# Kernel optimization log

Hardware: AMD Instinct MI355X
Metric: run time of the kernel (lower is better)

Reference implementation:

```python
import jax, jax.numpy as jnp
import numpy as np

N = 8192       # nodes
IN_F = 512     # in_features
OUT_F = 256    # out_features


def setup_inputs() -> dict:
    key = jax.random.key(0)
    k1, k2, k3, k4 = jax.random.split(key, 4)
    # xavier_uniform-like scales for params
    w_scale = 1.414 * (6.0 / (IN_F + OUT_F)) ** 0.5
    a_scale = 1.414 * (6.0 / (2 * OUT_F + 1)) ** 0.5
    x = jax.random.normal(k1, (N, IN_F), jnp.float32)
    W = jax.random.uniform(k2, (IN_F, OUT_F), jnp.float32, -w_scale, w_scale)
    a = jax.random.uniform(k3, (2 * OUT_F, 1), jnp.float32, -a_scale, a_scale)
    adj = jax.random.randint(k4, (N, N), 0, 2, jnp.int32)
    return {"x": x, "W": W, "a": a, "adj": adj}


def reference(x, W, a, adj):
    # h = x @ W : [N, OUT_F]
    h = x @ W
    f = W.shape[1]
    a1, a2 = a[:f], a[f:]          # each [OUT_F, 1]
    # Original builds a_input[i,j] = concat(h_i, h_j) then matmuls with a.
    # Equivalent decomposition: e[i,j] = h_i . a1 + h_j . a2
    e = (h @ a1) + (h @ a2).T      # [N, N]
    neg = jnp.float32(-9e15)
    attention = jnp.where(adj > 0, e, neg)   # no softmax in the original
    h_prime = attention @ h        # [N, OUT_F]
    return h_prime
```

## Files before the change

### kernel.cpp

```cpp
#include <hip/hip_runtime.h>


#define NEG_BIG (-9000000000000000.0f)
#define POS_BIG (9000000000000000.0f)

typedef __bf16 bf16x8 __attribute__((ext_vector_type(8)));
typedef float f32x16 __attribute__((ext_vector_type(16)));

static __device__ __forceinline__ unsigned short f2bf(float f) {
  unsigned u = __builtin_bit_cast(unsigned, f);
  u = u + 0x7FFFu + ((u >> 16) & 1u);
  return (unsigned short)(u >> 16);
}
static __device__ __forceinline__ float bfbits2f(unsigned hi16) {
  return __builtin_bit_cast(float, hi16 << 16);
}
static __device__ __forceinline__ unsigned pk2(float a, float b) {
  return (unsigned)f2bf(a) | ((unsigned)f2bf(b) << 16);
}
static __device__ __forceinline__ unsigned m2(int a, int b) {
  return (unsigned)(a + (b << 16)) * 0x3F80u;
}
static __device__ __forceinline__ bf16x8 asbf(int4 q) {
  return __builtin_bit_cast(bf16x8, q);
}
static __device__ __forceinline__ bf16x8 mfrag(int4 u, int4 v) {
  union { unsigned w[4]; bf16x8 f; } r;
  r.w[0] = m2(u.x, u.y); r.w[1] = m2(u.z, u.w);
  r.w[2] = m2(v.x, v.y); r.w[3] = m2(v.z, v.w);
  return r.f;
}
static __device__ __forceinline__ f32x16 mfma(bf16x8 a, int4 b, f32x16 c) {
  return __builtin_amdgcn_mfma_f32_32x32x16_bf16(a, asbf(b), c, 0, 0, 0);
}

__global__ void k1a_wt(const float* __restrict__ W, unsigned short* __restrict__ WT,
                       float* __restrict__ T) {
  const int i = blockIdx.x * 256 + threadIdx.x;
  const int k = i >> 8, n = i & 255;
  WT[n * 512 + k] = f2bf(W[i]);
  if (blockIdx.x == 0) T[threadIdx.x] = 0.f;
}

__global__ __launch_bounds__(256) void k1b_h(const float* __restrict__ x,
    const unsigned short* __restrict__ WT, unsigned short* __restrict__ hP) {
  const int t = threadIdx.x;
  const int w = t >> 6, l = t & 63, l31 = l & 31, lh = l >> 5;
  const int gw = blockIdx.x * 4 + w;
  const int mt = gw >> 3, nt = gw & 7;
  const int m0 = mt << 5, n0 = nt << 5;
  f32x16 acc;
  for (int i = 0; i < 16; ++i) acc[i] = 0.f;
  const float* xr = x + (size_t)(m0 + l31) * 512 + lh * 8;
  const unsigned short* wr = WT + (size_t)(n0 + l31) * 512 + lh * 8;
#pragma unroll 4
  for (int k0 = 0; k0 < 512; k0 += 16) {
    float4 xa = *(const float4*)(xr + k0);
    float4 xb = *(const float4*)(xr + k0 + 4);
    int4 wb = *(const int4*)(wr + k0);
    union { unsigned u[4]; bf16x8 v; } A;
    A.u[0] = pk2(xa.x, xa.y); A.u[1] = pk2(xa.z, xa.w);
    A.u[2] = pk2(xb.x, xb.y); A.u[3] = pk2(xb.z, xb.w);
    acc = __builtin_amdgcn_mfma_f32_32x32x16_bf16(A.v, asbf(wb), acc, 0, 0, 0);
  }
#pragma unroll
  for (int reg = 0; reg < 16; ++reg) {
    const int m = m0 + (reg & 3) + 8 * (reg >> 2) + 4 * lh;
    const int n = n0 + l31;
    hP[(size_t)(m >> 5) * 8192 + n * 32 + (m & 31)] = f2bf(acc[reg]);
  }
}

__global__ __launch_bounds__(256) void k2_colsum(const unsigned short* __restrict__ hP,
                                                 float* __restrict__ T) {
  const int t = threadIdx.x;
  const int g = blockIdx.x;
  float s = 0.f;
#pragma unroll
  for (int b = 0; b < 8; ++b) {
    const int4* p = (const int4*)(hP + (size_t)(g * 8 + b) * 8192 + t * 32);
    int4 q0 = p[0], q1 = p[1], q2 = p[2], q3 = p[3];
    const unsigned* u = (const unsigned*)&q0;
#pragma unroll
    for (int i = 0; i < 4; ++i) s += bfbits2f(u[i] & 0xFFFFu) + bfbits2f(u[i] >> 16);
    u = (const unsigned*)&q1;
#pragma unroll
    for (int i = 0; i < 4; ++i) s += bfbits2f(u[i] & 0xFFFFu) + bfbits2f(u[i] >> 16);
    u = (const unsigned*)&q2;
#pragma unroll
    for (int i = 0; i < 4; ++i) s += bfbits2f(u[i] & 0xFFFFu) + bfbits2f(u[i] >> 16);
    u = (const unsigned*)&q3;
#pragma unroll
    for (int i = 0; i < 4; ++i) s += bfbits2f(u[i] & 0xFFFFu) + bfbits2f(u[i] >> 16);
  }
  atomicAdd(&T[t], s);
}

__global__ void k2b_init(const float* __restrict__ T, float* __restrict__ out) {
  const int i = blockIdx.x * 256 + threadIdx.x;
  const int n4 = (i & 63) * 4;
  float4 tv = *(const float4*)(T + n4);
  float4 o;
  o.x = NEG_BIG * tv.x; o.y = NEG_BIG * tv.y;
  o.z = NEG_BIG * tv.z; o.w = NEG_BIG * tv.w;
  ((float4*)out)[i] = o;
}

__global__ __launch_bounds__(256, 4) void k3_att(const int* __restrict__ adj,
    const unsigned short* __restrict__ hP, float* __restrict__ out) {
  const int t = threadIdx.x;
  const int blk = blockIdx.x;
  const int s = blk & 7;
  const int rt = blk >> 3;
  const int w = t >> 6;
  const int l = t & 63;
  const int l31 = l & 31;
  const int lh = l >> 5;
  const int n0 = w << 6;

  const int r0 = rt * 64 + l31;
  const int* aR0 = adj + (size_t)r0 * 8192 + s * 1024 + lh * 8;
  const int* aR1 = aR0 + (size_t)32 * 8192;
  const unsigned short* hB = hP + (size_t)(s * 32) * 8192 + (n0 + l31) * 32 + lh * 8;

  f32x16 a00, a01, a10, a11;
  for (int i = 0; i < 16; ++i) { a00[i] = 0.f; a01[i] = 0.f; a10[i] = 0.f; a11[i] = 0.f; }

  for (int it = 0; it < 32; ++it) {
    const int4* q0 = (const int4*)(aR0 + it * 32);
    const int4* q1 = (const int4*)(aR1 + it * 32);
    const unsigned short* hb = hB + (size_t)it * 8192;
    int4 b00 = *(const int4*)(hb);
    int4 b01 = *(const int4*)(hb + 16);
    int4 b10 = *(const int4*)(hb + 1024);
    int4 b11 = *(const int4*)(hb + 1040);
    int4 u00a = q0[0], u00b = q0[1];
    int4 u10a = q1[0], u10b = q1[1];
    bf16x8 A00 = mfrag(u00a, u00b);
    bf16x8 A10 = mfrag(u10a, u10b);
    a00 = mfma(A00, b00, a00);
    a01 = mfma(A00, b10, a01);
    a10 = mfma(A10, b00, a10);
    a11 = mfma(A10, b10, a11);
    int4 u01a = q0[4], u01b = q0[5];
    int4 u11a = q1[4], u11b = q1[5];
    bf16x8 A01 = mfrag(u01a, u01b);
    bf16x8 A11 = mfrag(u11a, u11b);
    a00 = mfma(A01, b01, a00);
    a01 = mfma(A01, b11, a01);
    a10 = mfma(A11, b01, a10);
    a11 = mfma(A11, b11, a11);
  }

  const int rb0 = rt * 64 + 4 * lh;
  const int nn = n0 + l31;
#pragma unroll
  for (int reg = 0; reg < 16; ++reg) {
    const int ro = (reg & 3) + 8 * (reg >> 2);
    float* p = out + (size_t)(rb0 + ro) * 256 + nn;
    atomicAdd(p, POS_BIG * a00[reg]);
    atomicAdd(p + 32, POS_BIG * a01[reg]);
    float* p2 = p + 32 * 256;
    atomicAdd(p2, POS_BIG * a10[reg]);
    atomicAdd(p2 + 32, POS_BIG * a11[reg]);
  }
}

extern "C" void kernel_launch(void* const* d_in, const int* in_sizes, int n_in,
                              void* d_out, int out_size, void* d_ws, size_t ws_size,
                              hipStream_t stream) {
  const float* x = (const float*)d_in[0];
  const float* W = (const float*)d_in[1];
  const int* adj = (const int*)d_in[3];
  float* out = (float*)d_out;
  char* ws = (char*)d_ws;
  unsigned short* WT = (unsigned short*)(ws);
  unsigned short* hP = (unsigned short*)(ws + (1 << 20));
  float* T = (float*)(ws + (6 << 20));

  k1a_wt<<<512, 256, 0, stream>>>(W, WT, T);
  k1b_h<<<512, 256, 0, stream>>>(x, WT, hP);
  k2_colsum<<<32, 256, 0, stream>>>(hP, T);
  k2b_init<<<2048, 256, 0, stream>>>(T, out);
  k3_att<<<1024, 256, 0, stream>>>(adj, hP, out);
}
```

Before: 530.7 us.

## Stage adjacency tiles through double-buffered LDS in attention kernel, widen colsum grid

The attention kernel stops having each wave load and convert its own adjacency fragments from global memory. All threads now cooperatively load 64x64 adjacency tiles with coalesced loads, convert them once to bf16, and write them into a padded, double-buffered shared-memory tile that the waves read as MFMA A-fragments. The next tile is prefetched while MFMAs run on the current one. This removes the redundant global reads and conversions that the four waves each did for the same rows, at the cost of one barrier per iteration and extra LDS use that may limit occupancy. Separately, the column-sum kernel now uses one block per row-block, 256 blocks instead of 32, which increases parallelism but also the number of atomic adds.

```diff
diff --git a/kernel.cpp b/kernel.cpp
--- a/kernel.cpp
+++ b/kernel.cpp
@@ -23,12 +23,6 @@
 }
 static __device__ __forceinline__ bf16x8 asbf(int4 q) {
   return __builtin_bit_cast(bf16x8, q);
-}
-static __device__ __forceinline__ bf16x8 mfrag(int4 u, int4 v) {
-  union { unsigned w[4]; bf16x8 f; } r;
-  r.w[0] = m2(u.x, u.y); r.w[1] = m2(u.z, u.w);
-  r.w[2] = m2(v.x, v.y); r.w[3] = m2(v.z, v.w);
-  return r.f;
 }
 static __device__ __forceinline__ f32x16 mfma(bf16x8 a, int4 b, f32x16 c) {
   return __builtin_amdgcn_mfma_f32_32x32x16_bf16(a, asbf(b), c, 0, 0, 0);
@@ -74,24 +68,20 @@
 __global__ __launch_bounds__(256) void k2_colsum(const unsigned short* __restrict__ hP,
                                                  float* __restrict__ T) {
   const int t = threadIdx.x;
-  const int g = blockIdx.x;
+  const int b = blockIdx.x;
+  const int4* p = (const int4*)(hP + (size_t)b * 8192 + t * 32);
+  int4 q0 = p[0], q1 = p[1], q2 = p[2], q3 = p[3];
   float s = 0.f;
-#pragma unroll
-  for (int b = 0; b < 8; ++b) {
-    const int4* p = (const int4*)(hP + (size_t)(g * 8 + b) * 8192 + t * 32);
-    int4 q0 = p[0], q1 = p[1], q2 = p[2], q3 = p[3];
-    const unsigned* u = (const unsigned*)&q0;
-#pragma unroll
-    for (int i = 0; i < 4; ++i) s += bfbits2f(u[i] & 0xFFFFu) + bfbits2f(u[i] >> 16);
-    u = (const unsigned*)&q1;
-#pragma unroll
-    for (int i = 0; i < 4; ++i) s += bfbits2f(u[i] & 0xFFFFu) + bfbits2f(u[i] >> 16);
-    u = (const unsigned*)&q2;
-#pragma unroll
-    for (int i = 0; i < 4; ++i) s += bfbits2f(u[i] & 0xFFFFu) + bfbits2f(u[i] >> 16);
-    u = (const unsigned*)&q3;
-#pragma unroll
-    for (int i = 0; i < 4; ++i) s += bfbits2f(u[i] & 0xFFFFu) + bfbits2f(u[i] >> 16);
+  const unsigned* u0 = (const unsigned*)&q0;
+  const unsigned* u1 = (const unsigned*)&q1;
+  const unsigned* u2 = (const unsigned*)&q2;
+  const unsigned* u3 = (const unsigned*)&q3;
+#pragma unroll
+  for (int i = 0; i < 4; ++i) {
+    s += bfbits2f(u0[i] & 0xFFFFu) + bfbits2f(u0[i] >> 16);
+    s += bfbits2f(u1[i] & 0xFFFFu) + bfbits2f(u1[i] >> 16);
+    s += bfbits2f(u2[i] & 0xFFFFu) + bfbits2f(u2[i] >> 16);
+    s += bfbits2f(u3[i] & 0xFFFFu) + bfbits2f(u3[i] >> 16);
   }
   atomicAdd(&T[t], s);
 }
@@ -106,8 +96,10 @@
   ((float4*)out)[i] = o;
 }
 
+#define LSTR 68
 __global__ __launch_bounds__(256, 4) void k3_att(const int* __restrict__ adj,
     const unsigned short* __restrict__ hP, float* __restrict__ out) {
+  __shared__ unsigned short A[2][64 * LSTR];
   const int t = threadIdx.x;
   const int blk = blockIdx.x;
   const int s = blk & 7;
@@ -118,38 +110,71 @@
   const int lh = l >> 5;
   const int n0 = w << 6;
 
-  const int r0 = rt * 64 + l31;
-  const int* aR0 = adj + (size_t)r0 * 8192 + s * 1024 + lh * 8;
-  const int* aR1 = aR0 + (size_t)32 * 8192;
-  const unsigned short* hB = hP + (size_t)(s * 32) * 8192 + (n0 + l31) * 32 + lh * 8;
+  const int srow = t >> 4;
+  const int scol = (t & 15) << 2;
+  const int* aBase = adj + (size_t)(rt * 64 + srow) * 8192 + s * 1024 + scol;
+  unsigned short* const wA0 = &A[0][srow * LSTR + scol];
+  unsigned short* const wA1 = &A[1][srow * LSTR + scol];
+
+  const int fr0 = l31 * (LSTR * 2) + lh * 16;
+  const int fr1 = fr0 + 32 * (LSTR * 2);
+
+  const unsigned short* hB = hP + (n0 + l31) * 32 + lh * 8;
 
   f32x16 a00, a01, a10, a11;
   for (int i = 0; i < 16; ++i) { a00[i] = 0.f; a01[i] = 0.f; a10[i] = 0.f; a11[i] = 0.f; }
 
-  for (int it = 0; it < 32; ++it) {
-    const int4* q0 = (const int4*)(aR0 + it * 32);
-    const int4* q1 = (const int4*)(aR1 + it * 32);
-    const unsigned short* hb = hB + (size_t)it * 8192;
-    int4 b00 = *(const int4*)(hb);
-    int4 b01 = *(const int4*)(hb + 16);
-    int4 b10 = *(const int4*)(hb + 1024);
-    int4 b11 = *(const int4*)(hb + 1040);
-    int4 u00a = q0[0], u00b = q0[1];
-    int4 u10a = q1[0], u10b = q1[1];
-    bf16x8 A00 = mfrag(u00a, u00b);
-    bf16x8 A10 = mfrag(u10a, u10b);
-    a00 = mfma(A00, b00, a00);
-    a01 = mfma(A00, b10, a01);
-    a10 = mfma(A10, b00, a10);
-    a11 = mfma(A10, b10, a11);
-    int4 u01a = q0[4], u01b = q0[5];
-    int4 u11a = q1[4], u11b = q1[5];
-    bf16x8 A01 = mfrag(u01a, u01b);
-    bf16x8 A11 = mfrag(u11a, u11b);
-    a00 = mfma(A01, b01, a00);
-    a01 = mfma(A01, b11, a01);
-    a10 = mfma(A11, b01, a10);
-    a11 = mfma(A11, b11, a11);
+  {
+    int4 v0 = *(const int4*)(aBase);
+    int4 v1 = *(const int4*)(aBase + (size_t)16 * 8192);
+    int4 v2 = *(const int4*)(aBase + (size_t)32 * 8192);
+    int4 v3 = *(const int4*)(aBase + (size_t)48 * 8192);
+    *(uint2*)(wA0)             = make_uint2(m2(v0.x, v0.y), m2(v0.z, v0.w));
+    *(uint2*)(wA0 + 16 * LSTR) = make_uint2(m2(v1.x, v1.y), m2(v1.z, v1.w));
+    *(uint2*)(wA0 + 32 * LSTR) = make_uint2(m2(v2.x, v2.y), m2(v2.z, v2.w));
+    *(uint2*)(wA0 + 48 * LSTR) = make_uint2(m2(v3.x, v3.y), m2(v3.z, v3.w));
+  }
+
+  for (int it = 0; it < 16; ++it) {
+    __syncthreads();
+    int4 v0, v1, v2, v3;
+    if (it < 15) {
+      const int* ab = aBase + (it + 1) * 64;
+      v0 = *(const int4*)(ab);
+      v1 = *(const int4*)(ab + (size_t)16 * 8192);
+      v2 = *(const int4*)(ab + (size_t)32 * 8192);
+      v3 = *(const int4*)(ab + (size_t)48 * 8192);
+    }
+    const unsigned short* hb0 = hB + (size_t)(s * 32 + it * 2) * 8192;
+    const unsigned short* hb1 = hb0 + 8192;
+    int4 b00 = *(const int4*)(hb0);
+    int4 b01 = *(const int4*)(hb0 + 16);
+    int4 b0n = *(const int4*)(hb0 + 1024);
+    int4 b1n = *(const int4*)(hb0 + 1040);
+    int4 b20 = *(const int4*)(hb1);
+    int4 b21 = *(const int4*)(hb1 + 16);
+    int4 b2n = *(const int4*)(hb1 + 1024);
+    int4 b3n = *(const int4*)(hb1 + 1040);
+
+    const char* Ab = (const char*)&A[it & 1][0];
+#pragma unroll
+    for (int ks = 0; ks < 4; ++ks) {
+      bf16x8 A0 = *(const bf16x8*)(Ab + fr0 + ks * 32);
+      bf16x8 A1 = *(const bf16x8*)(Ab + fr1 + ks * 32);
+      int4 Bn0 = (ks == 0) ? b00 : (ks == 1) ? b01 : (ks == 2) ? b20 : b21;
+      int4 Bn1 = (ks == 0) ? b0n : (ks == 1) ? b1n : (ks == 2) ? b2n : b3n;
+      a00 = mfma(A0, Bn0, a00);
+      a01 = mfma(A0, Bn1, a01);
+      a10 = mfma(A1, Bn0, a10);
+      a11 = mfma(A1, Bn1, a11);
+    }
+    if (it < 15) {
+      unsigned short* wn = ((it & 1) ? wA0 : wA1);
+      *(uint2*)(wn)             = make_uint2(m2(v0.x, v0.y), m2(v0.z, v0.w));
+      *(uint2*)(wn + 16 * LSTR) = make_uint2(m2(v1.x, v1.y), m2(v1.z, v1.w));
+      *(uint2*)(wn + 32 * LSTR) = make_uint2(m2(v2.x, v2.y), m2(v2.z, v2.w));
+      *(uint2*)(wn + 48 * LSTR) = make_uint2(m2(v3.x, v3.y), m2(v3.z, v3.w));
+    }
   }
 
   const int rb0 = rt * 64 + 4 * lh;
@@ -180,7 +205,7 @@
 
   k1a_wt<<<512, 256, 0, stream>>>(W, WT, T);
   k1b_h<<<512, 256, 0, stream>>>(x, WT, hP);
-  k2_colsum<<<32, 256, 0, stream>>>(hP, T);
+  k2_colsum<<<256, 256, 0, stream>>>(hP, T);
   k2b_init<<<2048, 256, 0, stream>>>(T, out);
   k3_att<<<1024, 256, 0, stream>>>(adj, hP, out);
 }
```

Measured after the change: 476.8 us. -10.1%, faster.
